# Kernel tuning notes

Measured on AMD Instinct MI355X. Metric: run time of the kernel, lower is better.

Reference implementation:

```python
import jax, jax.numpy as jnp
import numpy as np

N, E, D, H, C = 40000, 640000, 128, 4, 32  # nodes, edges, in_hid, heads, out_channels/head
NUM_NODE_TYPE, NUM_EDGE_TYPE = 8, 8
NEG_SLOPE = 0.2
EDGE_TYPE_SELF = 0


def setup_inputs() -> dict:
    key = jax.random.key(0)
    ks = jax.random.split(key, 12)
    x = jax.random.normal(ks[0], (N, D), dtype=jnp.float32)
    # build edges with no self-loops (the module filters src==dst before adding self-loops)
    src = jax.random.randint(ks[1], (E,), 0, N, dtype=jnp.int32)
    off = jax.random.randint(ks[2], (E,), 1, N, dtype=jnp.int32)
    dst = (src + off) % N
    edge_index = jnp.stack([src, dst])  # [2, E]
    node_type = jax.random.randint(ks[3], (N,), 0, NUM_NODE_TYPE, dtype=jnp.int32)
    edge_type = jax.random.randint(ks[4], (E,), 0, NUM_EDGE_TYPE, dtype=jnp.int32)
    g = 0.05
    Wq = jax.random.normal(ks[5], (H * C, D), dtype=jnp.float32) * g
    Wk = jax.random.normal(ks[6], (H * C, D), dtype=jnp.float32) * g
    Wv = jax.random.normal(ks[7], (H * C, D), dtype=jnp.float32) * g
    att_i = jax.random.normal(ks[8], (1, H, C), dtype=jnp.float32) * g
    att_j = jax.random.normal(ks[9], (1, H, C), dtype=jnp.float32) * g
    bias = jnp.zeros((H * C,), dtype=jnp.float32)
    node_emb_table = jax.random.normal(ks[10], (NUM_NODE_TYPE, D), dtype=jnp.float32) * g
    edge_emb_table = jax.random.normal(ks[11], (NUM_EDGE_TYPE, D), dtype=jnp.float32) * g
    return {"x": x, "edge_index": edge_index, "node_type": node_type,
            "edge_type": edge_type, "Wq": Wq, "Wk": Wk, "Wv": Wv,
            "att_i": att_i, "att_j": att_j, "bias": bias,
            "node_emb_table": node_emb_table, "edge_emb_table": edge_emb_table}


def reference(x, edge_index, node_type, edge_type, Wq, Wk, Wv,
              att_i, att_j, bias, node_emb_table, edge_emb_table):
    n = x.shape[0]
    # node-type embedding add
    x = x + node_emb_table[node_type]                       # [N, D]
    xq = x @ Wq.T                                           # [N, H*C]
    # add self-loops (input edges contain no src==dst by construction)
    self_idx = jnp.arange(n, dtype=edge_index.dtype)
    src = jnp.concatenate([edge_index[0], self_idx])        # [E+N]
    dst = jnp.concatenate([edge_index[1], self_idx])        # [E+N]
    et = jnp.concatenate([edge_type,
                          jnp.full((n,), EDGE_TYPE_SELF, dtype=edge_type.dtype)])
    edge_emb = edge_emb_table[et]                           # [E+N, D]
    # message: per-edge gather + K/V linear + additive attention
    x_j = x[src] + edge_emb                                 # [E+N, D]
    xq_i = xq[dst].reshape(-1, H, C)                        # [E+N, H, C]
    x_k = (x_j @ Wk.T).reshape(-1, H, C)
    x_v = (x_j @ Wv.T).reshape(-1, H, C)
    alpha = (xq_i * att_i).sum(-1) + (x_k * att_j).sum(-1)  # [E+N, H]
    alpha = jax.nn.leaky_relu(alpha, NEG_SLOPE)
    # segment softmax over destination nodes (PyG softmax, eps=1e-16)
    amax = jax.ops.segment_max(alpha, dst, num_segments=n)  # [N, H]
    alpha = jnp.exp(alpha - amax[dst])
    denom = jax.ops.segment_sum(alpha, dst, num_segments=n)
    alpha = alpha / (denom[dst] + 1e-16)
    # scatter-add weighted values
    out = jax.ops.segment_sum(x_v * alpha[..., None], dst, num_segments=n)  # [N, H, C]
    return out.reshape(n, H * C) + bias
```

## Files before the change

kernel.cpp:

```cpp
#include <hip/hip_runtime.h>
#include <math.h>

#define NN 40000
#define NE 640000
#define D 128
#define NH 4
#define NC 32
#define NEG 0.2f

typedef __attribute__((ext_vector_type(8))) short bf16x8;
typedef __attribute__((ext_vector_type(4))) float f32x4;

__device__ __forceinline__ unsigned pack_bf16(float a, float b) {
  unsigned ua = __float_as_uint(a), ub = __float_as_uint(b);
  ua = (ua + 0x7FFFu + ((ua >> 16) & 1u)) >> 16;
  ub = (ub + 0x7FFFu + ((ub >> 16) & 1u)) & 0xFFFF0000u;
  return ub | ua;
}

__device__ __forceinline__ bf16x8 to_bf16x8(float4 a, float4 b) {
  union { bf16x8 v; unsigned u[4]; } r;
  r.u[0] = pack_bf16(a.x, a.y);
  r.u[1] = pack_bf16(a.z, a.w);
  r.u[2] = pack_bf16(b.x, b.y);
  r.u[3] = pack_bf16(b.z, b.w);
  return r.v;
}

__device__ __forceinline__ float4 f4add(float4 a, float4 b) {
  return make_float4(a.x + b.x, a.y + b.y, a.z + b.z, a.w + b.w);
}

__global__ __launch_bounds__(256) void k_tables(
    const float* __restrict__ Wq, const float* __restrict__ Wk,
    const float* __restrict__ Wv,
    const float* __restrict__ att_i, const float* __restrict__ att_j,
    const float* __restrict__ eemb,
    float* __restrict__ ev, float* __restrict__ a_et,
    unsigned* __restrict__ Wvh, int* __restrict__ counts) {
  __shared__ float sm[1024];
  int b = blockIdx.x, t = threadIdx.x;
  if (b == 0) {
    for (int j = t; j < 1024; j += 256) {
      int isq = (j < 512);
      int h = (j >> 7) & 3, d = j & 127;
      const float* __restrict__ Wm = isq ? Wq : Wk;
      const float* __restrict__ am = isq ? att_i : att_j;
      float s = 0.f;
#pragma unroll
      for (int c = 0; c < NC; ++c) s = fmaf(am[h * NC + c], Wm[(h * NC + c) * D + d], s);
      sm[j] = s;
    }
    __syncthreads();
    for (int j = t; j < 1024; j += 256) {
      int r = j >> 6;
      int c2 = (j & 63) * 2;
      float a = 0.f, bb = 0.f;
      if (r < 8) { a = sm[r * 128 + c2]; bb = sm[r * 128 + c2 + 1]; }
      Wvh[(128 + r) * 64 + (j & 63)] = pack_bf16(a, bb);
    }
    if (t < 32) {
      int ty = t >> 2, hh = t & 3;
      const float* wrow = sm + 512 + hh * 128;
      const float* __restrict__ emb = eemb + ty * D;
      float s = 0.f;
#pragma unroll 8
      for (int d = 0; d < D; ++d) s = fmaf(wrow[d], emb[d], s);
      a_et[t] = s;
    }
  } else if (b <= 8) {
    int ty = b - 1;
    if (t < 128) sm[t] = eemb[ty * D + t];
    __syncthreads();
    if (t < 128) {
      const float4* __restrict__ wr = (const float4*)(Wv + (size_t)t * D);
      const float4* __restrict__ er = (const float4*)sm;
      float s = 0.f;
#pragma unroll
      for (int k = 0; k < 32; ++k) {
        float4 ww = wr[k], ee = er[k];
        s = fmaf(ww.x, ee.x, s); s = fmaf(ww.y, ee.y, s);
        s = fmaf(ww.z, ee.z, s); s = fmaf(ww.w, ee.w, s);
      }
      ev[ty * D + t] = s;
    }
  } else if (b <= 16) {
    int j0 = (b - 9) * 1024;
    for (int j = j0 + t; j < j0 + 1024; j += 256)
      Wvh[j] = pack_bf16(Wv[2 * j], Wv[2 * j + 1]);
  } else {
    int i = (b - 17) * 256 + t;
    if (i < NN / 4) ((int4*)counts)[i] = make_int4(0, 0, 0, 0);
  }
}

__global__ __launch_bounds__(256) void k_sxi(
    const int* __restrict__ ei, const int* __restrict__ etype,
    int* __restrict__ counts, unsigned* __restrict__ packed,
    const float* __restrict__ x, const int* __restrict__ node_type,
    const float* __restrict__ nemb, const unsigned* __restrict__ Wvh,
    unsigned* __restrict__ xvh, float* __restrict__ aq, float* __restrict__ ak) {
  int b = blockIdx.x, t = threadIdx.x;
  if (b % 5 != 0) {
    int sb = b - (b + 4) / 5;
    int i = sb * 256 + t;
    int src = ei[i];
    int dst = ei[NE + i];
    int et  = etype[i];
    int r = atomicAdd(&counts[dst], 1);
    if (r < 63) packed[(dst << 6) + r] = (unsigned)src | ((unsigned)et << 16);
    return;
  }
  int bb = b / 5;
  int w = t >> 6, l = t & 63;
  int quad = l >> 4, col = l & 15;
  int n0w = bb * 64 + w * 16;
  int node = n0w + col;
  int ntA = node_type[node];
  const float4* __restrict__ xr = (const float4*)(x + (size_t)node * D);
  const float4* __restrict__ nr = (const float4*)(nemb + (size_t)ntA * D);
  bf16x8 afr[4];
#pragma unroll
  for (int s = 0; s < 4; ++s) {
    const float4* p = xr + s * 8 + quad * 2;
    const float4* q4 = nr + s * 8 + quad * 2;
    afr[s] = to_bf16x8(f4add(p[0], q4[0]), f4add(p[1], q4[1]));
  }
  f32x4 acc[9];
#pragma unroll
  for (int ct = 0; ct < 9; ++ct) acc[ct] = (f32x4){0.f, 0.f, 0.f, 0.f};
#pragma unroll
  for (int ct = 0; ct < 9; ++ct) {
    const unsigned* __restrict__ brow = Wvh + (size_t)(ct * 16 + col) * 64;
#pragma unroll
    for (int s = 0; s < 4; ++s) {
      bf16x8 bfr = *(const bf16x8*)(brow + s * 16 + quad * 4);
      acc[ct] = __builtin_amdgcn_mfma_f32_16x16x32_bf16(afr[s], bfr, acc[ct], 0, 0, 0);
    }
  }
  int nodes[4];
#pragma unroll
  for (int r = 0; r < 4; ++r) nodes[r] = n0w + quad * 4 + r;
#pragma unroll
  for (int ct = 0; ct < 8; ++ct) {
#pragma unroll
    for (int r = 0; r < 4; ++r) {
      float val = acc[ct][r];
      float pv = __shfl_xor(val, 1);
      if (!(col & 1)) {
        xvh[nodes[r] * 64 + ct * 8 + (col >> 1)] = pack_bf16(val, pv);
      }
    }
  }
  if (col < 4) {
#pragma unroll
    for (int r = 0; r < 4; ++r) aq[nodes[r] * NH + col] = acc[8][r];
  } else if (col < 8) {
#pragma unroll
    for (int r = 0; r < 4; ++r) ak[nodes[r] * NH + (col - 4)] = acc[8][r];
  }
}

__global__ __launch_bounds__(256) void k_gather(const int* __restrict__ counts,
        const unsigned* __restrict__ packed,
        const float* __restrict__ aq, const float* __restrict__ ak,
        const float* __restrict__ a_et, const unsigned* __restrict__ xvh,
        const float* __restrict__ ev, const float* __restrict__ bias,
        float* __restrict__ out) {
  int n = (int)((blockIdx.x * blockDim.x + threadIdx.x) >> 6);
  int l = threadIdx.x & 63;
  if (n >= NN) return;
  int g = l >> 3, q = l & 7;
  int h = q >> 1;
  float aqh = aq[n * NH + h];
  int e0 = n << 6;
  int deg = min(counts[n], 63);
  int m = deg + 1;
  const uint4* __restrict__ xv4 = (const uint4*)xvh;
  float acc[16];
#pragma unroll
  for (int k = 0; k < 16; ++k) acc[k] = 0.f;
  float ps[8];
#pragma unroll
  for (int k = 0; k < 8; ++k) ps[k] = 0.f;
  int iters = (m + 7) >> 3;
  int i = g;
  bool val = (i < m);
  unsigned rec = (val && i < deg) ? packed[e0 + i] : (unsigned)n;
  int src = (int)(rec & 0xFFFFu), etc = (int)(rec >> 16);
  float sA = ak[src * NH + h] + a_et[etc * NH + h];
  uint4 vb0 = xv4[src * 16 + 2 * q];
  uint4 vb1 = xv4[src * 16 + 2 * q + 1];
  for (int it = 0; it < iters; ++it) {
    int i2 = i + 8;
    bool v2 = (i2 < m);
    float sAn = 0.f; int etn = 0;
    uint4 vb0n = make_uint4(0, 0, 0, 0), vb1n = make_uint4(0, 0, 0, 0);
    if (it + 1 < iters) {
      unsigned rec2 = (v2 && i2 < deg) ? packed[e0 + i2] : (unsigned)n;
      int s2 = (int)(rec2 & 0xFFFFu);
      etn = (int)(rec2 >> 16);
      sAn = ak[s2 * NH + h] + a_et[etn * NH + h];
      vb0n = xv4[s2 * 16 + 2 * q];
      vb1n = xv4[s2 * 16 + 2 * q + 1];
    }
    float s = aqh + sA;
    s = (s > 0.f) ? s : NEG * s;
    float p = val ? __expf(s) : 0.f;
#pragma unroll
    for (int tt = 0; tt < 8; ++tt) ps[tt] += (etc == tt) ? p : 0.f;
    float f[16];
    f[0]  = __uint_as_float(vb0.x << 16); f[1]  = __uint_as_float(vb0.x & 0xFFFF0000u);
    f[2]  = __uint_as_float(vb0.y << 16); f[3]  = __uint_as_float(vb0.y & 0xFFFF0000u);
    f[4]  = __uint_as_float(vb0.z << 16); f[5]  = __uint_as_float(vb0.z & 0xFFFF0000u);
    f[6]  = __uint_as_float(vb0.w << 16); f[7]  = __uint_as_float(vb0.w & 0xFFFF0000u);
    f[8]  = __uint_as_float(vb1.x << 16); f[9]  = __uint_as_float(vb1.x & 0xFFFF0000u);
    f[10] = __uint_as_float(vb1.y << 16); f[11] = __uint_as_float(vb1.y & 0xFFFF0000u);
    f[12] = __uint_as_float(vb1.z << 16); f[13] = __uint_as_float(vb1.z & 0xFFFF0000u);
    f[14] = __uint_as_float(vb1.w << 16); f[15] = __uint_as_float(vb1.w & 0xFFFF0000u);
#pragma unroll
    for (int k = 0; k < 16; ++k) acc[k] = fmaf(p, f[k], acc[k]);
    i = i2; val = v2; sA = sAn; etc = etn; vb0 = vb0n; vb1 = vb1n;
  }
#pragma unroll
  for (int tt = 0; tt < 8; ++tt) {
    ps[tt] += __shfl_xor(ps[tt], 8);
    ps[tt] += __shfl_xor(ps[tt], 16);
    ps[tt] += __shfl_xor(ps[tt], 32);
  }
  float dsum = ((ps[0] + ps[1]) + (ps[2] + ps[3])) + ((ps[4] + ps[5]) + (ps[6] + ps[7]));
  float psg = ps[0];
#pragma unroll
  for (int tt = 1; tt < 8; ++tt) psg = (g == tt) ? ps[tt] : psg;
  const float4* __restrict__ ep = (const float4*)(ev + g * D + 16 * q);
  float4 ea0 = ep[0], ea1 = ep[1], ea2 = ep[2], ea3 = ep[3];
  acc[0]  = fmaf(psg, ea0.x, acc[0]);
  acc[1]  = fmaf(psg, ea0.y, acc[1]);
  acc[2]  = fmaf(psg, ea0.z, acc[2]);
  acc[3]  = fmaf(psg, ea0.w, acc[3]);
  acc[4]  = fmaf(psg, ea1.x, acc[4]);
  acc[5]  = fmaf(psg, ea1.y, acc[5]);
  acc[6]  = fmaf(psg, ea1.z, acc[6]);
  acc[7]  = fmaf(psg, ea1.w, acc[7]);
  acc[8]  = fmaf(psg, ea2.x, acc[8]);
  acc[9]  = fmaf(psg, ea2.y, acc[9]);
  acc[10] = fmaf(psg, ea2.z, acc[10]);
  acc[11] = fmaf(psg, ea2.w, acc[11]);
  acc[12] = fmaf(psg, ea3.x, acc[12]);
  acc[13] = fmaf(psg, ea3.y, acc[13]);
  acc[14] = fmaf(psg, ea3.z, acc[14]);
  acc[15] = fmaf(psg, ea3.w, acc[15]);
#pragma unroll
  for (int k = 0; k < 16; ++k) {
    acc[k] += __shfl_xor(acc[k], 8);
    acc[k] += __shfl_xor(acc[k], 16);
    acc[k] += __shfl_xor(acc[k], 32);
  }
  if (g == 0) {
    float inv = 1.f / (dsum + 1e-16f);
    const float4* __restrict__ b4 = (const float4*)(bias + 16 * q);
    float4* __restrict__ op = (float4*)(out + (size_t)n * D + 16 * q);
#pragma unroll
    for (int k4 = 0; k4 < 4; ++k4) {
      float4 bb = b4[k4];
      op[k4] = make_float4(acc[4 * k4 + 0] * inv + bb.x,
                           acc[4 * k4 + 1] * inv + bb.y,
                           acc[4 * k4 + 2] * inv + bb.z,
                           acc[4 * k4 + 3] * inv + bb.w);
    }
  }
}

extern "C" void kernel_launch(void* const* d_in, const int* in_sizes, int n_in,
                              void* d_out, int out_size, void* d_ws, size_t ws_size,
                              hipStream_t stream) {
  const float* x      = (const float*)d_in[0];
  const int*   ei     = (const int*)d_in[1];
  const int*   ntype  = (const int*)d_in[2];
  const int*   etype  = (const int*)d_in[3];
  const float* Wq     = (const float*)d_in[4];
  const float* Wk     = (const float*)d_in[5];
  const float* Wv     = (const float*)d_in[6];
  const float* att_i  = (const float*)d_in[7];
  const float* att_j  = (const float*)d_in[8];
  const float* bias   = (const float*)d_in[9];
  const float* nemb   = (const float*)d_in[10];
  const float* eemb   = (const float*)d_in[11];
  float* out = (float*)d_out;

  float* ws     = (float*)d_ws;
  unsigned* xvh = (unsigned*)ws;
  float* aq     = ws + (size_t)NN * 64;
  float* ak     = aq + NN * NH;
  float* ev     = ak + NN * NH;
  float* a_et   = ev + 1024;
  unsigned* Wvh = (unsigned*)(a_et + 32);
  int*   counts = (int*)(Wvh + 9216);
  unsigned* packed = (unsigned*)(counts + NN);

  k_tables<<<dim3(64), dim3(256), 0, stream>>>(Wq, Wk, Wv, att_i, att_j, eemb,
                                               ev, a_et, Wvh, counts);
  k_sxi<<<dim3(3125), dim3(256), 0, stream>>>(ei, etype, counts, packed,
                                              x, ntype, nemb, Wvh, xvh, aq, ak);
  k_gather<<<dim3((NN + 3) / 4), dim3(256), 0, stream>>>(counts, packed, aq, ak, a_et,
                                                         xvh, ev, bias, out);
}
```

Baseline: 176.4 us.

## Replace global per-node atomic CSR build with two-pass bucketed binning

```diff
diff --git a/kernel.cpp b/kernel.cpp
--- a/kernel.cpp
+++ b/kernel.cpp
@@ -7,6 +7,9 @@
 #define NH 4
 #define NC 32
 #define NEG 0.2f
+
+#define NBKT 625
+#define BIN_CAP 1536
 
 typedef __attribute__((ext_vector_type(8))) short bf16x8;
 typedef __attribute__((ext_vector_type(4))) float f32x4;
@@ -37,10 +40,11 @@
     const float* __restrict__ att_i, const float* __restrict__ att_j,
     const float* __restrict__ eemb,
     float* __restrict__ ev, float* __restrict__ a_et,
-    unsigned* __restrict__ Wvh, int* __restrict__ counts) {
+    unsigned* __restrict__ Wvh, int* __restrict__ btail) {
   __shared__ float sm[1024];
   int b = blockIdx.x, t = threadIdx.x;
   if (b == 0) {
+    for (int j = t; j < NBKT; j += 256) btail[j] = 0;
     for (int j = t; j < 1024; j += 256) {
       int isq = (j < 512);
       int h = (j >> 7) & 3, d = j & 127;
@@ -84,34 +88,56 @@
       }
       ev[ty * D + t] = s;
     }
-  } else if (b <= 16) {
+  } else {
     int j0 = (b - 9) * 1024;
     for (int j = j0 + t; j < j0 + 1024; j += 256)
       Wvh[j] = pack_bf16(Wv[2 * j], Wv[2 * j + 1]);
-  } else {
-    int i = (b - 17) * 256 + t;
-    if (i < NN / 4) ((int4*)counts)[i] = make_int4(0, 0, 0, 0);
   }
 }
 
 __global__ __launch_bounds__(256) void k_sxi(
     const int* __restrict__ ei, const int* __restrict__ etype,
-    int* __restrict__ counts, unsigned* __restrict__ packed,
+    int* __restrict__ btail, unsigned* __restrict__ binbuf,
     const float* __restrict__ x, const int* __restrict__ node_type,
     const float* __restrict__ nemb, const unsigned* __restrict__ Wvh,
     unsigned* __restrict__ xvh, float* __restrict__ aq, float* __restrict__ ak) {
   int b = blockIdx.x, t = threadIdx.x;
-  if (b % 5 != 0) {
-    int sb = b - (b + 4) / 5;
-    int i = sb * 256 + t;
-    int src = ei[i];
-    int dst = ei[NE + i];
-    int et  = etype[i];
-    int r = atomicAdd(&counts[dst], 1);
-    if (r < 63) packed[(dst << 6) + r] = (unsigned)src | ((unsigned)et << 16);
+  if (b % 9 == 0) {
+    int sb = b / 9;
+    __shared__ int hist[NBKT];
+    __shared__ int base[NBKT];
+    for (int j = t; j < NBKT; j += 256) hist[j] = 0;
+    __syncthreads();
+    int e0 = sb * 8192;
+    for (int k = 0; k < 32; ++k) {
+      int e = e0 + k * 256 + t;
+      if (e < NE) atomicAdd(&hist[ei[NE + e] >> 6], 1);
+    }
+    __syncthreads();
+    for (int j = t; j < NBKT; j += 256) {
+      int h = hist[j];
+      base[j] = h ? atomicAdd(&btail[j], h) : 0;
+    }
+    __syncthreads();
+    for (int j = t; j < NBKT; j += 256) hist[j] = 0;
+    __syncthreads();
+    for (int k = 0; k < 32; ++k) {
+      int e = e0 + k * 256 + t;
+      if (e < NE) {
+        int src = ei[e];
+        int dst = ei[NE + e];
+        int et  = etype[e];
+        int bk = dst >> 6;
+        int r = atomicAdd(&hist[bk], 1);
+        int p = base[bk] + r;
+        if (p < BIN_CAP)
+          binbuf[bk * BIN_CAP + p] =
+              (unsigned)src | ((unsigned)et << 16) | ((unsigned)(dst & 63) << 19);
+      }
+    }
     return;
   }
-  int bb = b / 5;
+  int bb = b - b / 9 - 1;
   int w = t >> 6, l = t & 63;
   int quad = l >> 4, col = l & 15;
   int n0w = bb * 64 + w * 16;
@@ -159,6 +185,30 @@
 #pragma unroll
     for (int r = 0; r < 4; ++r) ak[nodes[r] * NH + (col - 4)] = acc[8][r];
   }
+}
+
+__global__ __launch_bounds__(256) void k_binb(
+    const int* __restrict__ btail, const unsigned* __restrict__ binbuf,
+    int* __restrict__ counts, unsigned* __restrict__ packed) {
+  __shared__ int lcnt[64];
+  __shared__ unsigned csr[4096];
+  int b = blockIdx.x, t = threadIdx.x;
+  if (t < 64) lcnt[t] = 0;
+  __syncthreads();
+  int cnt = btail[b];
+  if (cnt > BIN_CAP) cnt = BIN_CAP;
+  const unsigned* __restrict__ bp = binbuf + (size_t)b * BIN_CAP;
+  for (int j = t; j < cnt; j += 256) {
+    unsigned rec = bp[j];
+    int loc = (int)(rec >> 19) & 63;
+    int r = atomicAdd(&lcnt[loc], 1);
+    if (r < 63) csr[(loc << 6) + r] = rec & 0x7FFFFu;
+  }
+  __syncthreads();
+  if (t < 64) counts[(b << 6) + t] = lcnt[t];
+  int4* __restrict__ pp = (int4*)(packed + (size_t)b * 4096);
+  const int4* __restrict__ cs = (const int4*)csr;
+  for (int j = t; j < 1024; j += 256) pp[j] = cs[j];
 }
 
 __global__ __launch_bounds__(256) void k_gather(const int* __restrict__ counts,
@@ -297,11 +347,14 @@
   unsigned* Wvh = (unsigned*)(a_et + 32);
   int*   counts = (int*)(Wvh + 9216);
   unsigned* packed = (unsigned*)(counts + NN);
-
-  k_tables<<<dim3(64), dim3(256), 0, stream>>>(Wq, Wk, Wv, att_i, att_j, eemb,
-                                               ev, a_et, Wvh, counts);
-  k_sxi<<<dim3(3125), dim3(256), 0, stream>>>(ei, etype, counts, packed,
-                                              x, ntype, nemb, Wvh, xvh, aq, ak);
+  int* btail    = (int*)(packed + (size_t)NN * 64);
+  unsigned* binbuf = (unsigned*)(btail + 640);
+
+  k_tables<<<dim3(17), dim3(256), 0, stream>>>(Wq, Wk, Wv, att_i, att_j, eemb,
+                                               ev, a_et, Wvh, btail);
+  k_sxi<<<dim3(704), dim3(256), 0, stream>>>(ei, etype, btail, binbuf,
+                                             x, ntype, nemb, Wvh, xvh, aq, ak);
+  k_binb<<<dim3(NBKT), dim3(256), 0, stream>>>(btail, binbuf, counts, packed);
   k_gather<<<dim3((NN + 3) / 4), dim3(256), 0, stream>>>(counts, packed, aq, ak, a_et,
                                                          xvh, ev, bias, out);
 }
```

Result: no change. 174.8 us (-0.9%).
